# Kernel tuning notes

Hardware: AMD Instinct MI355X
Metric: run time of the kernel (lower is better)

## Reference

```python
import jax, jax.numpy as jnp
import numpy as np

NUM_DENSE = 13
NUM_SPARSE = 26
FEAT_NUM = 40000  # categories per sparse field
FEATURE_LENGTH = NUM_SPARSE * FEAT_NUM + NUM_DENSE  # 1_040_013
K = 64
BATCH = 4096


def setup_inputs() -> dict:
    key = jax.random.key(0)
    k1, k2, k3, k4 = jax.random.split(key, 4)
    dense_inputs = jax.random.normal(k1, (BATCH, NUM_DENSE), dtype=jnp.float32)
    sparse_inputs = jax.random.randint(k2, (BATCH, NUM_SPARSE), 0, FEAT_NUM, dtype=jnp.int64)
    w0 = jnp.zeros((1,), dtype=jnp.float32)
    w = jax.random.normal(k3, (FEATURE_LENGTH, 1), dtype=jnp.float32) * 0.05
    V = jax.random.normal(k4, (K, FEATURE_LENGTH), dtype=jnp.float32) * 0.05
    return {"dense_inputs": dense_inputs, "sparse_inputs": sparse_inputs, "w0": w0, "w": w, "V": V}


def reference(dense_inputs, sparse_inputs, w0, w, V):
    # Feature layout matches the original concat order: [dense (NUM_DENSE) | one-hot field 0 | ... | one-hot field 25].
    # The one-hot @ matrix products are computed as row gathers (mathematically identical,
    # since one_hot(i) @ M == M[i]).
    offsets = NUM_DENSE + FEAT_NUM * jnp.arange(NUM_SPARSE, dtype=sparse_inputs.dtype)
    idx = sparse_inputs + offsets[None, :]  # [B, NUM_SPARSE] global row ids into feature_length

    # ---- first order: w0 + stack @ w ----
    w_dense = w[:NUM_DENSE]            # [ND, 1]
    first = w0 + dense_inputs @ w_dense + jnp.sum(w[idx, 0], axis=1, keepdims=True)  # [B,1]

    # ---- second order: 0.5 * sum((stack @ V^T)^2 - (stack^2 @ (V^T)^2), axis=1) ----
    Vt = V.T                           # [F, K]
    Vt_dense = Vt[:NUM_DENSE]          # [ND, K]
    Vt_sparse = Vt[idx]                # [B, NUM_SPARSE, K] gathered latent vectors

    sv = dense_inputs @ Vt_dense + jnp.sum(Vt_sparse, axis=1)                 # [B, K]
    # stack^2 for the one-hot block equals the one-hot block itself (0/1 entries)
    s2v2 = (dense_inputs ** 2) @ (Vt_dense ** 2) + jnp.sum(Vt_sparse ** 2, axis=1)  # [B, K]

    second = 0.5 * jnp.sum(sv ** 2 - s2v2, axis=1, keepdims=True)  # [B,1]
    return first + second
```

## Files before the change

### kernel.cpp

```cpp
#include <hip/hip_runtime.h>

#define NUM_DENSE 13
#define NUM_SPARSE 26
#define FEAT_NUM 40000
#define FEATURE_LENGTH (NUM_SPARSE * FEAT_NUM + NUM_DENSE)
#define KDIM 64
#define BATCH 4096

__global__ void idx_kernel(const int* __restrict__ sp, int* __restrict__ idx32) {
    int tid = blockIdx.x * blockDim.x + threadIdx.x;
    int j = tid >> 12;
    int b = tid & 4095;
    idx32[tid] = NUM_DENSE + j * FEAT_NUM + sp[b * NUM_SPARSE + j];
}

__global__ __launch_bounds__(1024) void accum_kernel(const float* __restrict__ V,
                                                     const int* __restrict__ idx32,
                                                     float* __restrict__ S,
                                                     float* __restrict__ Q) {
    const int k = blockIdx.x;
    const int b = blockIdx.y * 1024 + threadIdx.x;
    const float* __restrict__ Vk = V + (size_t)k * FEATURE_LENGTH;
    float s = 0.f, q = 0.f;
#pragma unroll
    for (int j = 0; j < NUM_SPARSE; ++j) {
        int i = idx32[j * BATCH + b];
        float v = Vk[i];
        s += v;
        q += v * v;
    }
    S[k * BATCH + b] = s;
    Q[k * BATCH + b] = q;
}

__global__ void final_kernel(const float* __restrict__ dense,
                             const float* __restrict__ w0,
                             const float* __restrict__ w,
                             const float* __restrict__ V,
                             const int* __restrict__ idx32,
                             const float* __restrict__ S,
                             const float* __restrict__ Q,
                             float* __restrict__ out) {
    const int wave = threadIdx.x >> 6;
    const int lane = threadIdx.x & 63;
    const int b = blockIdx.x * 4 + wave;
    const int k = lane;
    const float* __restrict__ Vk = V + (size_t)k * FEATURE_LENGTH;

    float sv = S[k * BATCH + b];
    float qv = Q[k * BATCH + b];
#pragma unroll
    for (int d = 0; d < NUM_DENSE; ++d) {
        float x  = dense[b * NUM_DENSE + d];
        float vv = Vk[d];
        sv += x * vv;
        qv += x * x * vv * vv;
    }
    float t = 0.5f * (sv * sv - qv);

    if (lane < NUM_SPARSE) t += w[idx32[lane * BATCH + b]];
    if (lane >= 32 && lane < 32 + NUM_DENSE) {
        int d = lane - 32;
        t += dense[b * NUM_DENSE + d] * w[d];
    }

#pragma unroll
    for (int off = 32; off > 0; off >>= 1) t += __shfl_down(t, off);
    if (lane == 0) out[b] = w0[0] + t;
}

extern "C" void kernel_launch(void* const* d_in, const int* in_sizes, int n_in,
                              void* d_out, int out_size, void* d_ws, size_t ws_size,
                              hipStream_t stream) {
    const float* dense  = (const float*)d_in[0];
    const int*   sparse = (const int*)d_in[1];
    const float* w0     = (const float*)d_in[2];
    const float* w      = (const float*)d_in[3];
    const float* V      = (const float*)d_in[4];
    float* out = (float*)d_out;

    char* ws = (char*)d_ws;
    int*   idx32 = (int*)ws;
    float* S     = (float*)(ws + (1 << 19));
    float* Q     = (float*)(ws + (1 << 19) + BATCH * KDIM * 4);

    idx_kernel<<<(NUM_SPARSE * BATCH) / 256, 256, 0, stream>>>(sparse, idx32);
    accum_kernel<<<dim3(KDIM, 4), 1024, 0, stream>>>(V, idx32, S, Q);
    final_kernel<<<BATCH / 4, 256, 0, stream>>>(dense, w0, w, V, idx32, S, Q, out);
}
```

Baseline: 414.4 us.

## Stream V field segments through LDS windows instead of random global gathers

Result: no change. 406.9 us (-1.8%).

```diff
diff --git a/kernel.cpp b/kernel.cpp
--- a/kernel.cpp
+++ b/kernel.cpp
@@ -6,40 +6,85 @@
 #define FEATURE_LENGTH (NUM_SPARSE * FEAT_NUM + NUM_DENSE)
 #define KDIM 64
 #define BATCH 4096
+#define QSIZE 10000
+#define NT 1024
 
-__global__ void idx_kernel(const int* __restrict__ sp, int* __restrict__ idx32) {
+__global__ void transpose_kernel(const int* __restrict__ sp, int* __restrict__ sp_t) {
     int tid = blockIdx.x * blockDim.x + threadIdx.x;
     int j = tid >> 12;
     int b = tid & 4095;
-    idx32[tid] = NUM_DENSE + j * FEAT_NUM + sp[b * NUM_SPARSE + j];
+    sp_t[tid] = sp[b * NUM_SPARSE + j];
 }
 
-__global__ __launch_bounds__(1024) void accum_kernel(const float* __restrict__ V,
-                                                     const int* __restrict__ idx32,
-                                                     float* __restrict__ S,
-                                                     float* __restrict__ Q) {
+__global__ __launch_bounds__(NT) void accum_kernel(const float* __restrict__ V,
+                                                   const int* __restrict__ sp_t,
+                                                   float* __restrict__ PS,
+                                                   float* __restrict__ PQ) {
+    __shared__ __align__(16) float win[QSIZE + 4];
+
     const int k = blockIdx.x;
-    const int b = blockIdx.y * 1024 + threadIdx.x;
-    const float* __restrict__ Vk = V + (size_t)k * FEATURE_LENGTH;
-    float s = 0.f, q = 0.f;
+    const int g = blockIdx.y;
+    const int jstart = g * 7 - (g > 2 ? (g - 2) : 0);
+    const int jend   = jstart + (g < 2 ? 7 : 6);
+    const int tid = threadIdx.x;
+
+    float sAcc[4] = {0.f, 0.f, 0.f, 0.f};
+    float qAcc[4] = {0.f, 0.f, 0.f, 0.f};
+
+    for (int j = jstart; j < jend; ++j) {
+        int spv[4];
 #pragma unroll
-    for (int j = 0; j < NUM_SPARSE; ++j) {
-        int i = idx32[j * BATCH + b];
-        float v = Vk[i];
-        s += v;
-        q += v * v;
+        for (int r = 0; r < 4; ++r) spv[r] = sp_t[j * BATCH + tid + NT * r];
+
+        for (int q = 0; q < 4; ++q) {
+            const size_t s0 = (size_t)k * FEATURE_LENGTH + NUM_DENSE
+                            + (size_t)j * FEAT_NUM + q * QSIZE;
+            const float* __restrict__ Vq = V + s0;
+            const int h   = (4 - ((int)(s0 & 3))) & 3;
+            const int off = (4 - h) & 3;
+            const int n4  = (QSIZE - h) >> 2;
+            const int tl  = (QSIZE - h) & 3;
+
+            __syncthreads();
+            if (tid < h) win[off + tid] = Vq[tid];
+            const float4* __restrict__ Vq4 = (const float4*)(Vq + h);
+            for (int m = tid; m < n4; m += NT) {
+                float4 v = Vq4[m];
+                *reinterpret_cast<float4*>(&win[off + h + 4 * m]) = v;
+            }
+            const int ts = h + 4 * n4;
+            if (tid < tl) win[off + ts + tid] = Vq[ts + tid];
+            __syncthreads();
+
+            const int q0 = q * QSIZE;
+#pragma unroll
+            for (int r = 0; r < 4; ++r) {
+                int rel = spv[r] - q0;
+                bool in = (rel >= 0) && (rel < QSIZE);
+                int a = in ? (rel + off) : 0;
+                float v = win[a];
+                v = in ? v : 0.f;
+                sAcc[r] += v;
+                qAcc[r] += v * v;
+            }
+        }
     }
-    S[k * BATCH + b] = s;
-    Q[k * BATCH + b] = q;
+
+    const int base = (g * KDIM + k) * BATCH + tid;
+#pragma unroll
+    for (int r = 0; r < 4; ++r) {
+        PS[base + NT * r] = sAcc[r];
+        PQ[base + NT * r] = qAcc[r];
+    }
 }
 
 __global__ void final_kernel(const float* __restrict__ dense,
                              const float* __restrict__ w0,
                              const float* __restrict__ w,
                              const float* __restrict__ V,
-                             const int* __restrict__ idx32,
-                             const float* __restrict__ S,
-                             const float* __restrict__ Q,
+                             const int* __restrict__ sp_t,
+                             const float* __restrict__ PS,
+                             const float* __restrict__ PQ,
                              float* __restrict__ out) {
     const int wave = threadIdx.x >> 6;
     const int lane = threadIdx.x & 63;
@@ -47,8 +92,12 @@
     const int k = lane;
     const float* __restrict__ Vk = V + (size_t)k * FEATURE_LENGTH;
 
-    float sv = S[k * BATCH + b];
-    float qv = Q[k * BATCH + b];
+    float sv = 0.f, qv = 0.f;
+#pragma unroll
+    for (int g = 0; g < 4; ++g) {
+        sv += PS[(g * KDIM + k) * BATCH + b];
+        qv += PQ[(g * KDIM + k) * BATCH + b];
+    }
 #pragma unroll
     for (int d = 0; d < NUM_DENSE; ++d) {
         float x  = dense[b * NUM_DENSE + d];
@@ -58,7 +107,8 @@
     }
     float t = 0.5f * (sv * sv - qv);
 
-    if (lane < NUM_SPARSE) t += w[idx32[lane * BATCH + b]];
+    if (lane < NUM_SPARSE)
+        t += w[NUM_DENSE + lane * FEAT_NUM + sp_t[lane * BATCH + b]];
     if (lane >= 32 && lane < 32 + NUM_DENSE) {
         int d = lane - 32;
         t += dense[b * NUM_DENSE + d] * w[d];
@@ -80,11 +130,11 @@
     float* out = (float*)d_out;
 
     char* ws = (char*)d_ws;
-    int*   idx32 = (int*)ws;
-    float* S     = (float*)(ws + (1 << 19));
-    float* Q     = (float*)(ws + (1 << 19) + BATCH * KDIM * 4);
+    int*   sp_t = (int*)ws;
+    float* PS   = (float*)(ws + (1 << 19));
+    float* PQ   = (float*)(ws + (1 << 19) + 4 * KDIM * BATCH * 4);
 
-    idx_kernel<<<(NUM_SPARSE * BATCH) / 256, 256, 0, stream>>>(sparse, idx32);
-    accum_kernel<<<dim3(KDIM, 4), 1024, 0, stream>>>(V, idx32, S, Q);
-    final_kernel<<<BATCH / 4, 256, 0, stream>>>(dense, w0, w, V, idx32, S, Q, out);
+    transpose_kernel<<<(NUM_SPARSE * BATCH) / 256, 256, 0, stream>>>(sparse, sp_t);
+    accum_kernel<<<dim3(KDIM, 4), NT, 0, stream>>>(V, sp_t, PS, PQ);
+    final_kernel<<<BATCH / 4, 256, 0, stream>>>(dense, w0, w, V, sp_t, PS, PQ, out);
 }
```
